# Kernel tuning notes

Hardware: AMD Instinct MI355X
Metric: run time of the kernel (lower is better)

Reference implementation:

```python
import jax, jax.numpy as jnp
import numpy as np

RADIUS = 1.0
BUMP = 32          # config.bump_steps
SCALE = 100.0      # sigmoid sharpness in compute_ecc
G = 32             # num_graphs

N, E, F = 16000, 48000, 32000
DIM, NDIR = 3, 64
HID, NC = 256, 10


def compute_ecc(h, index, lin):
    # h: [M, D]; lin: [BUMP] thresholds; index: [M] graph ids
    # sigmoid(scale * (lin - h)) broadcast -> [M, BUMP, D], segment-sum over M
    ecc = jax.nn.sigmoid(SCALE * (lin[None, :, None] - h[:, None, :]))
    return jax.ops.segment_sum(ecc, index, num_segments=G)  # [G, BUMP, D]


def setup_inputs() -> dict:
    key = jax.random.key(0)
    ks = jax.random.split(key, 12)
    x = jax.random.normal(ks[0], (N, DIM), dtype=jnp.float32)
    node_weights = jax.random.uniform(ks[1], (N,), dtype=jnp.float32)
    edge_weights = jax.random.uniform(ks[2], (E,), dtype=jnp.float32)
    face_weights = jax.random.uniform(ks[3], (F,), dtype=jnp.float32)
    v = jax.random.normal(ks[4], (DIM, NDIR), dtype=jnp.float32)
    v = v / jnp.linalg.norm(v, axis=0, keepdims=True)  # unit directions
    W1 = jax.random.normal(ks[5], (HID, NDIR * BUMP), dtype=jnp.float32) * 0.02
    b1 = jnp.zeros((HID,), dtype=jnp.float32)
    W2 = jax.random.normal(ks[6], (NC, HID), dtype=jnp.float32) * 0.02
    b2 = jnp.zeros((NC,), dtype=jnp.float32)
    edge_index = jax.random.randint(ks[7], (2, E), 0, N, dtype=jnp.int64)
    face = jax.random.randint(ks[8], (3, F), 0, N, dtype=jnp.int64)
    batch_ids = jnp.sort(jax.random.randint(ks[9], (N,), 0, G, dtype=jnp.int64))
    return {"x": x, "node_weights": node_weights, "edge_weights": edge_weights,
            "face_weights": face_weights, "v": v, "W1": W1, "b1": b1,
            "W2": W2, "b2": b2, "edge_index": edge_index, "face": face,
            "batch_ids": batch_ids}


def reference(x, node_weights, edge_weights, face_weights, v, W1, b1, W2, b2,
              edge_index, face, batch_ids):
    lin = jnp.linspace(-RADIUS, RADIUS, BUMP, dtype=jnp.float32)
    # node heights: weighted coords projected onto directions -> [N, D]
    nh = (x * node_weights[:, None]) @ v
    # edge heights: max over the 2 endpoints, then weight -> [E, D]
    eh = jnp.maximum(nh[edge_index[0]], nh[edge_index[1]]) * edge_weights[:, None]
    idx_e = batch_ids[edge_index[0]]
    # face heights: max over the 3 vertices -> [F, D]
    fh = jnp.max(nh[face], axis=0) * face_weights[:, None]
    idx_f = batch_ids[face[0]]
    ecc = compute_ecc(nh, batch_ids, lin)   # [G, BUMP, D]
    ecc = ecc - compute_ecc(eh, idx_e, lin)
    ecc = ecc + compute_ecc(fh, idx_f, lin)
    flat = ecc.reshape(G, -1)               # [G, BUMP*D]
    h = jax.nn.relu(flat @ W1.T + b1)
    logits = h @ W2.T + b2
    return (logits, flat)
```

## Files before the change

kernel.cpp:

```cpp
#include <hip/hip_runtime.h>
#include <hip/hip_bf16.h>

constexpr int NN = 16000, NE = 48000, NF = 32000;
constexpr int ND = 64, NB = 32, NG = 32;
constexpr int HIDN = 256, NCLS = 10;
constexpr int CHB = 32;
constexpr int EFB = (NE + NF + 255) / 256;
constexpr int PREB = EFB;
constexpr int CAPE = 4096, CAPF = 4096;
constexpr float KLOG = 144.26950408889634f;
constexpr float DLT  = 9.307710457348151f;
constexpr float INV_DLT = 0.10743849569269015f;
constexpr int HBINS = 39;

constexpr int ECCF_OFF = 0;
constexpr int CUR_OFF  = ECCF_OFF + NG * NB * ND;
constexpr int NOFS_OFF = CUR_OFF + 64;
constexpr int DONE_OFF = NOFS_OFF + 40;
constexpr int ER_OFF   = DONE_OFF + 32;
constexpr int FR_OFF   = ER_OFF + NG * CAPE * 8;
constexpr int HB_OFF   = FR_OFF + NG * CAPF * 12;
constexpr int ZERO_CNT = NG * NB * ND;

__device__ __forceinline__ int clamp_node(int n) {
    return ((unsigned)n < (unsigned)NN) ? n : 0;
}
template<bool BF> __device__ __forceinline__ float ldf(const void* p, int i) {
    return BF ? __bfloat162float(((const __hip_bfloat16*)p)[i]) : ((const float*)p)[i];
}
template<bool I64> __device__ __forceinline__ int ldi(const int* p, int i) {
    return I64 ? p[2 * i] : p[i];
}

__device__ __forceinline__ bool detect_bf(const void* xp) {
    const unsigned* xw = (const unsigned*)xp;
    unsigned w = xw[threadIdx.x & 63];
    return __ballot(((w >> 23) & 0xFFu) >= 200u) != 0ull;
}
__device__ __forceinline__ bool detect_i64(const int* eip) {
    const unsigned* eiw = (const unsigned*)eip;
    unsigned o = eiw[2 * (threadIdx.x & 63) + 1];
    return __ballot(o != 0u) == 0ull;
}

__device__ __forceinline__ float dot3w(float4 p, float v0, float v1, float v2) {
    return fmaf(p.z, v2, fmaf(p.y, v1, p.x * v0));
}

__device__ __forceinline__ void accum_hist(float h, float s, float* hb) {
    const float KDEC = __builtin_amdgcn_exp2f(-DLT);
    float hkL = fmaf(h, KLOG, KLOG);
    float fl = floorf((hkL - 14.0f) * INV_DLT);
    int jlo = (int)fl + 1;
    if (jlo >= 32) return;
    if (jlo < -4) { hb[4 * 64] += s; return; }
    float t0 = fmaf(-(fl + 1.0f), DLT, hkL);
    float e  = __builtin_amdgcn_exp2f(t0);
    float s0 = __builtin_amdgcn_rcpf(1.0f + e);  e *= KDEC;
    float s1 = __builtin_amdgcn_rcpf(1.0f + e);  e *= KDEC;
    float s2 = __builtin_amdgcn_rcpf(1.0f + e);
    float* p = hb + (jlo + 4) * 64;
    float v0 = p[0], v1 = p[64], v2 = p[128], v3 = p[192];
    p[0]   = v0 + s * s0;
    p[64]  = v1 + s * (s1 - s0);
    p[128] = v2 + s * (s2 - s1);
    p[192] = v3 + s * (1.0f - s2);
}

template<bool BF, bool I64>
__device__ __forceinline__ void pre_body(const void* x, const void* nw,
                                         const int* ei, const int* fc, const int* batch,
                                         const void* ew, const void* fw,
                                         float* wsf, int* wsi, unsigned* cur,
                                         float4* er4, float4* fr4,
                                         unsigned* cnt, unsigned* base) {
    int t = threadIdx.x;
    int gid = blockIdx.x * 256 + t;

    if (gid < ZERO_CNT / 4) {
        float4 z; z.x = z.y = z.z = z.w = 0.0f;
        *(float4*)(wsf + ECCF_OFF + gid * 4) = z;
    }

    if (blockIdx.x == 0 && t < 32)
        ((unsigned*)wsi)[DONE_OFF + t] = 0u;

    if (gid < NN) {
        int gn = ldi<I64>(batch, gid) & (NG - 1);
        int gp = (gid > 0) ? (ldi<I64>(batch, gid - 1) & (NG - 1)) : -1;
        for (int gg = gp + 1; gg <= gn; gg++) wsi[NOFS_OFF + gg] = gid;
        if (gid == NN - 1)
            for (int gg = gn + 1; gg <= NG; gg++) wsi[NOFS_OFF + gg] = NN;
    }

    {
        if (t < 64) cnt[t] = 0;
        __syncthreads();
        int id = gid;
        int bin = 0; unsigned rank = 0; bool act = false;
        if (id < NE + NF) {
            if (id < NE) bin = ldi<I64>(batch, clamp_node(ldi<I64>(ei, id))) & 31;
            else bin = 32 + (ldi<I64>(batch, clamp_node(ldi<I64>(fc, id - NE))) & 31);
            act = true;
            rank = atomicAdd(&cnt[bin], 1u);
        }
        __syncthreads();
        if (t < 64) base[t] = cnt[t] ? atomicAdd(&cur[t], cnt[t]) : 0u;
        __syncthreads();
        if (act) {
            int off = (int)(base[bin] + rank);
            if (bin < 32) {
                if (off < CAPE) {
                    int a = clamp_node(ldi<I64>(ei, id));
                    int b = clamp_node(ldi<I64>(ei, NE + id));
                    float wa = ldf<BF>(nw, a), wb = ldf<BF>(nw, b);
                    float4 ra, rb;
                    ra.x = ldf<BF>(x, 3*a)   * wa;
                    ra.y = ldf<BF>(x, 3*a+1) * wa;
                    ra.z = ldf<BF>(x, 3*a+2) * wa;
                    ra.w = ldf<BF>(ew, id);
                    rb.x = ldf<BF>(x, 3*b)   * wb;
                    rb.y = ldf<BF>(x, 3*b+1) * wb;
                    rb.z = ldf<BF>(x, 3*b+2) * wb;
                    rb.w = 0.0f;
                    float4* dst = er4 + ((size_t)bin * CAPE + off) * 2;
                    dst[0] = ra; dst[1] = rb;
                }
            } else {
                if (off < CAPF) {
                    int fid = id - NE;
                    int a = clamp_node(ldi<I64>(fc, fid));
                    int b = clamp_node(ldi<I64>(fc, NF + fid));
                    int c = clamp_node(ldi<I64>(fc, 2 * NF + fid));
                    float wa = ldf<BF>(nw, a), wb = ldf<BF>(nw, b), wc = ldf<BF>(nw, c);
                    float4 qa, qb, qc;
                    qa.x = ldf<BF>(x, 3*a)   * wa;
                    qa.y = ldf<BF>(x, 3*a+1) * wa;
                    qa.z = ldf<BF>(x, 3*a+2) * wa;
                    qa.w = ldf<BF>(fw, fid);
                    qb.x = ldf<BF>(x, 3*b)   * wb;
                    qb.y = ldf<BF>(x, 3*b+1) * wb;
                    qb.z = ldf<BF>(x, 3*b+2) * wb;
                    qb.w = 0.0f;
                    qc.x = ldf<BF>(x, 3*c)   * wc;
                    qc.y = ldf<BF>(x, 3*c+1) * wc;
                    qc.z = ldf<BF>(x, 3*c+2) * wc;
                    qc.w = 0.0f;
                    float4* dst = fr4 + ((size_t)(bin - 32) * CAPF + off) * 3;
                    dst[0] = qa; dst[1] = qb; dst[2] = qc;
                }
            }
        }
    }
}
__global__ __launch_bounds__(256) void k_pre(const void* __restrict__ x,
                                             const void* __restrict__ nw,
                                             const int* __restrict__ ei,
                                             const int* __restrict__ fc,
                                             const int* __restrict__ batch,
                                             const void* __restrict__ ew,
                                             const void* __restrict__ fw,
                                             float* __restrict__ wsf,
                                             int* __restrict__ wsi,
                                             unsigned* __restrict__ cur,
                                             float4* __restrict__ er4,
                                             float4* __restrict__ fr4) {
    __shared__ unsigned cnt[64], base[64];
    bool bf = detect_bf(x), i64 = detect_i64(ei);
    if (bf)  { if (i64) pre_body<true,true >(x,nw,ei,fc,batch,ew,fw,wsf,wsi,cur,er4,fr4,cnt,base);
               else     pre_body<true,false>(x,nw,ei,fc,batch,ew,fw,wsf,wsi,cur,er4,fr4,cnt,base); }
    else     { if (i64) pre_body<false,true >(x,nw,ei,fc,batch,ew,fw,wsf,wsi,cur,er4,fr4,cnt,base);
               else     pre_body<false,false>(x,nw,ei,fc,batch,ew,fw,wsf,wsi,cur,er4,fr4,cnt,base); }
}

template<bool BF>
__device__ __forceinline__ void ecc_body(const void* xx, const void* nw, const void* vv,
                                         const int* wsi, const unsigned* cur,
                                         float* eccf, const float4* er4,
                                         const float4* fr4, float* hist) {
    int t = threadIdx.x;
    int d = t & 63;
    int w = __builtin_amdgcn_readfirstlane(t) >> 6;
    int g  = blockIdx.x >> 5;
    int cb = blockIdx.x & (CHB - 1);
    int sid = cb * 4 + w;
    const int S = CHB * 4;

    float v0 = ldf<BF>(vv, d), v1 = ldf<BF>(vv, ND + d), v2 = ldf<BF>(vv, 2 * ND + d);

    float4* h4 = (float4*)hist;
    const int Q = HBINS * 16;
    float4 z; z.x = z.y = z.z = z.w = 0.0f;
    for (int j = t; j < 4 * Q; j += 256) h4[j] = z;
    __syncthreads();

    float* hb = hist + w * (HBINS * 64) + d;

    int ns = wsi[NOFS_OFF + g], nend = wsi[NOFS_OFF + g + 1];
    int i = ns + sid;
    for (; i + S < nend; i += 2 * S) {
        int j = i + S;
        float a0 = ldf<BF>(xx, 3*i), a1 = ldf<BF>(xx, 3*i+1), a2 = ldf<BF>(xx, 3*i+2);
        float wa = ldf<BF>(nw, i);
        float b0 = ldf<BF>(xx, 3*j), b1 = ldf<BF>(xx, 3*j+1), b2 = ldf<BF>(xx, 3*j+2);
        float wb = ldf<BF>(nw, j);
        accum_hist(fmaf(a2, v2, fmaf(a1, v1, a0 * v0)) * wa, 1.0f, hb);
        accum_hist(fmaf(b2, v2, fmaf(b1, v1, b0 * v0)) * wb, 1.0f, hb);
    }
    for (; i < nend; i += S) {
        float a0 = ldf<BF>(xx, 3*i), a1 = ldf<BF>(xx, 3*i+1), a2 = ldf<BF>(xx, 3*i+2);
        float wa = ldf<BF>(nw, i);
        accum_hist(fmaf(a2, v2, fmaf(a1, v1, a0 * v0)) * wa, 1.0f, hb);
    }

    int ecnt = min((int)cur[g], CAPE);
    const float4* eg = er4 + (size_t)g * CAPE * 2;
    i = sid;
    for (; i + S < ecnt; i += 2 * S) {
        float4 pa1 = eg[2*i],       pb1 = eg[2*i + 1];
        float4 pa2 = eg[2*(i+S)],   pb2 = eg[2*(i+S) + 1];
        float h1 = fmaxf(dot3w(pa1, v0, v1, v2), dot3w(pb1, v0, v1, v2)) * pa1.w;
        float h2 = fmaxf(dot3w(pa2, v0, v1, v2), dot3w(pb2, v0, v1, v2)) * pa2.w;
        accum_hist(h1, -1.0f, hb);
        accum_hist(h2, -1.0f, hb);
    }
    for (; i < ecnt; i += S) {
        float4 pa = eg[2*i], pb = eg[2*i + 1];
        accum_hist(fmaxf(dot3w(pa, v0, v1, v2), dot3w(pb, v0, v1, v2)) * pa.w,
                   -1.0f, hb);
    }

    int fcnt = min((int)cur[32 + g], CAPF);
    const float4* fg = fr4 + (size_t)g * CAPF * 3;
    i = sid;
    for (; i + S < fcnt; i += 2 * S) {
        float4 qa1 = fg[3*i], qb1 = fg[3*i + 1], qc1 = fg[3*i + 2];
        float4 qa2 = fg[3*(i+S)], qb2 = fg[3*(i+S) + 1], qc2 = fg[3*(i+S) + 2];
        float h1 = fmaxf(fmaxf(dot3w(qa1, v0, v1, v2), dot3w(qb1, v0, v1, v2)),
                         dot3w(qc1, v0, v1, v2)) * qa1.w;
        float h2 = fmaxf(fmaxf(dot3w(qa2, v0, v1, v2), dot3w(qb2, v0, v1, v2)),
                         dot3w(qc2, v0, v1, v2)) * qa2.w;
        accum_hist(h1, 1.0f, hb);
        accum_hist(h2, 1.0f, hb);
    }
    for (; i < fcnt; i += S) {
        float4 qa = fg[3*i], qb = fg[3*i + 1], qc = fg[3*i + 2];
        accum_hist(fmaxf(fmaxf(dot3w(qa, v0, v1, v2), dot3w(qb, v0, v1, v2)),
                         dot3w(qc, v0, v1, v2)) * qa.w, 1.0f, hb);
    }

    __syncthreads();
    for (int o = t; o < Q; o += 256) {
        float4 A = h4[o], B = h4[Q + o], C = h4[2*Q + o], D = h4[3*Q + o];
        A.x += B.x + C.x + D.x;  A.y += B.y + C.y + D.y;
        A.z += B.z + C.z + D.z;  A.w += B.w + C.w + D.w;
        h4[o] = A;
    }
    __syncthreads();
    {
        float* segw = hist + HBINS * 64;
        float run = 0.0f, pre[8];
#pragma unroll
        for (int jj = 0; jj < 8; jj++) {
            run += hist[(4 + w * 8 + jj) * 64 + d];
            pre[jj] = run;
        }
        float padb = hist[d] + hist[64 + d] + hist[128 + d] + hist[192 + d];
        segw[w * 64 + d] = run;
        __syncthreads();
        float base = padb;
#pragma unroll
        for (int u = 0; u < 3; u++) if (u < w) base += segw[u * 64 + d];
        float* eb = eccf + g * (NB * ND) + d;
#pragma unroll
        for (int jj = 0; jj < 8; jj++)
            unsafeAtomicAdd(eb + (w * 8 + jj) * 64, base + pre[jj]);
    }
}
__global__ __launch_bounds__(256, 4) void k_ecc(const void* __restrict__ x,
                                                const void* __restrict__ nw,
                                                const void* __restrict__ v,
                                                const int* __restrict__ wsi,
                                                const unsigned* __restrict__ cur,
                                                float* __restrict__ eccf,
                                                const float4* __restrict__ er4,
                                                const float4* __restrict__ fr4) {
    __shared__ float hist[4 * HBINS * 64];
    if (detect_bf(x)) ecc_body<true >(x, nw, v, wsi, cur, eccf, er4, fr4, hist);
    else              ecc_body<false>(x, nw, v, wsi, cur, eccf, er4, fr4, hist);
}

template<bool BF>
__device__ __forceinline__ void mlp_body(const void* W1, const void* b1,
                                         const void* W2, const void* b2,
                                         const float* eccf, float* hbuf,
                                         unsigned* done, void* outv,
                                         float* red, float* pr, unsigned* lastflag) {
    int g = blockIdx.x >> 3, hc = blockIdx.x & 7;
    int t = threadIdx.x;

    const float4* fp = (const float4*)(eccf + g * (NB * ND) + t * 8);
    float4 fa = fp[0], fb = fp[1];
    float fl[8] = {fa.x, fa.y, fa.z, fa.w, fb.x, fb.y, fb.z, fb.w};

    if (hc == 0) {
        int ob = NG * NCLS + g * (NB * ND) + t * 8;
        if (BF) {
#pragma unroll
            for (int j = 0; j < 8; j++)
                ((__hip_bfloat16*)outv)[ob + j] = __float2bfloat16(fl[j]);
        } else {
            ((float4*)((float*)outv + ob))[0] = fa;
            ((float4*)((float*)outv + ob))[1] = fb;
        }
    }

    float acc[32];
#pragma unroll
    for (int r = 0; r < 32; r++) acc[r] = 0.0f;
#pragma unroll 4
    for (int r = 0; r < 32; r++) {
        size_t wb = (size_t)(hc * 32 + r) * (NB * ND) + t * 8;
        float wv[8];
        if (BF) {
            uint4 u = *(const uint4*)((const __hip_bfloat16*)W1 + wb);
            wv[0] = __uint_as_float(u.x << 16); wv[1] = __uint_as_float(u.x & 0xffff0000u);
            wv[2] = __uint_as_float(u.y << 16); wv[3] = __uint_as_float(u.y & 0xffff0000u);
            wv[4] = __uint_as_float(u.z << 16); wv[5] = __uint_as_float(u.z & 0xffff0000u);
            wv[6] = __uint_as_float(u.w << 16); wv[7] = __uint_as_float(u.w & 0xffff0000u);
        } else {
            float4 a = *(const float4*)((const float*)W1 + wb);
            float4 b = *(const float4*)((const float*)W1 + wb + 4);
            wv[0]=a.x; wv[1]=a.y; wv[2]=a.z; wv[3]=a.w;
            wv[4]=b.x; wv[5]=b.y; wv[6]=b.z; wv[7]=b.w;
        }
        float s = 0.0f;
#pragma unroll
        for (int j = 0; j < 8; j++) s = fmaf(wv[j], fl[j], s);
        acc[r] = s;
    }

#pragma unroll
    for (int r = 0; r < 32; r++) red[t * 33 + r] = acc[r];
    __syncthreads();
    {
        int r = t >> 3, s8 = t & 7;
        float sum = 0.0f;
#pragma unroll
        for (int i = 0; i < 32; i++) sum += red[(s8 * 32 + i) * 33 + r];
        pr[r * 8 + s8] = sum;
    }
    __syncthreads();
    if (t < 32) {
        float h = ldf<BF>(b1, hc * 32 + t);
#pragma unroll
        for (int s8 = 0; s8 < 8; s8++) h += pr[t * 8 + s8];
        __hip_atomic_store(&hbuf[g * HIDN + hc * 32 + t], fmaxf(h, 0.0f),
                           __ATOMIC_RELAXED, __HIP_MEMORY_SCOPE_AGENT);
    }

    __syncthreads();
    if (t == 0) {
        unsigned prev = __hip_atomic_fetch_add(&done[g], 1u, __ATOMIC_RELAXED,
                                               __HIP_MEMORY_SCOPE_AGENT);
        *lastflag = (prev == 7u) ? 1u : 0u;
    }
    __syncthreads();
    if (*lastflag) {
        red[t] = __hip_atomic_load(&hbuf[g * HIDN + t], __ATOMIC_RELAXED,
                                   __HIP_MEMORY_SCOPE_AGENT);
        __syncthreads();
        int w = t >> 6, lane = t & 63;
        for (int c = w; c < NCLS; c += 4) {
            float p = red[lane]        * ldf<BF>(W2, c * HIDN + lane)
                    + red[lane + 64]   * ldf<BF>(W2, c * HIDN + lane + 64)
                    + red[lane + 128]  * ldf<BF>(W2, c * HIDN + lane + 128)
                    + red[lane + 192]  * ldf<BF>(W2, c * HIDN + lane + 192);
#pragma unroll
            for (int off = 32; off >= 1; off >>= 1) p += __shfl_xor(p, off);
            if (lane == 0) {
                float r = p + ldf<BF>(b2, c);
                if (BF) ((__hip_bfloat16*)outv)[g * NCLS + c] = __float2bfloat16(r);
                else    ((float*)outv)[g * NCLS + c] = r;
            }
        }
    }
}
__global__ __launch_bounds__(256) void k_mlp(const void* __restrict__ W1,
                                             const void* __restrict__ b1,
                                             const void* __restrict__ W2,
                                             const void* __restrict__ b2,
                                             const float* __restrict__ eccf,
                                             float* __restrict__ hbuf,
                                             unsigned* __restrict__ done,
                                             void* __restrict__ outv,
                                             const void* __restrict__ x) {
    __shared__ float red[256 * 33];
    __shared__ float pr[256];
    __shared__ unsigned lastflag;
    if (detect_bf(x)) mlp_body<true >(W1, b1, W2, b2, eccf, hbuf, done, outv, red, pr, &lastflag);
    else              mlp_body<false>(W1, b1, W2, b2, eccf, hbuf, done, outv, red, pr, &lastflag);
}

extern "C" void kernel_launch(void* const* d_in, const int* in_sizes, int n_in,
                              void* d_out, int out_size, void* d_ws, size_t ws_size,
                              hipStream_t stream) {
    const void* x  = d_in[0];
    const void* nw = d_in[1];
    const void* ew = d_in[2];
    const void* fw = d_in[3];
    const void* v  = d_in[4];
    const void* W1 = d_in[5];
    const void* b1 = d_in[6];
    const void* W2 = d_in[7];
    const void* b2 = d_in[8];
    const int* ei    = (const int*)d_in[9];
    const int* fc    = (const int*)d_in[10];
    const int* batch = (const int*)d_in[11];

    float*    wsf = (float*)d_ws;
    unsigned* wsu = (unsigned*)d_ws;
    int*      wsi = (int*)d_ws;
    float*    eccf = wsf + ECCF_OFF;
    unsigned* cur  = wsu + CUR_OFF;
    unsigned* done = wsu + DONE_OFF;
    float*    hbuf = wsf + HB_OFF;
    float4*   er4  = (float4*)(wsf + ER_OFF);
    float4*   fr4  = (float4*)(wsf + FR_OFF);

    hipMemsetAsync((char*)d_ws + (size_t)CUR_OFF * 4, 0, 64 * 4, stream);

    k_pre<<<PREB, 256, 0, stream>>>(x, nw, ei, fc, batch, ew, fw, wsf, wsi, cur, er4, fr4);
    k_ecc<<<NG * CHB, 256, 0, stream>>>(x, nw, v, wsi, cur, eccf, er4, fr4);
    k_mlp<<<NG * 8, 256, 0, stream>>>(W1, b1, W2, b2, eccf, hbuf, done, d_out, x);
}
```

Measured before the change: 118.6 us.

## Fuse MLP stage into ECC kernel with per-graph completion counter spin-wait

Removes the separate MLP kernel launch. Each ECC block drains its atomics and bumps a per-graph done counter. The first 8 chunk blocks of each graph then spin until all 32 blocks have finished and run the MLP chunk, reusing the histogram shared memory. The counters are now cleared by a wider memset, and a second counter handles the final-layer reduction. This relies on all 1024 blocks being co-resident to avoid deadlock, and it adds spin-wait latency on the critical blocks.

```diff
diff --git a/kernel.cpp b/kernel.cpp
--- a/kernel.cpp
+++ b/kernel.cpp
@@ -17,10 +17,12 @@
 constexpr int CUR_OFF  = ECCF_OFF + NG * NB * ND;
 constexpr int NOFS_OFF = CUR_OFF + 64;
 constexpr int DONE_OFF = NOFS_OFF + 40;
-constexpr int ER_OFF   = DONE_OFF + 32;
+constexpr int DONE2_OFF= DONE_OFF + 32;
+constexpr int ER_OFF   = DONE2_OFF + 32;
 constexpr int FR_OFF   = ER_OFF + NG * CAPE * 8;
 constexpr int HB_OFF   = FR_OFF + NG * CAPF * 12;
 constexpr int ZERO_CNT = NG * NB * ND;
+constexpr int MS_WORDS = 168;
 
 __device__ __forceinline__ int clamp_node(int n) {
     return ((unsigned)n < (unsigned)NN) ? n : 0;
@@ -81,9 +83,6 @@
         float4 z; z.x = z.y = z.z = z.w = 0.0f;
         *(float4*)(wsf + ECCF_OFF + gid * 4) = z;
     }
-
-    if (blockIdx.x == 0 && t < 32)
-        ((unsigned*)wsi)[DONE_OFF + t] = 0u;
 
     if (gid < NN) {
         int gn = ldi<I64>(batch, gid) & (NG - 1);
@@ -174,134 +173,20 @@
 }
 
 template<bool BF>
-__device__ __forceinline__ void ecc_body(const void* xx, const void* nw, const void* vv,
-                                         const int* wsi, const unsigned* cur,
-                                         float* eccf, const float4* er4,
-                                         const float4* fr4, float* hist) {
+__device__ __forceinline__ void mlp_chunk(int g, int hc, const void* W1, const void* b1,
+                                          const void* W2, const void* b2,
+                                          const float* eccf, float* hbuf,
+                                          unsigned* done2, void* outv,
+                                          float* red, float* pr, unsigned* lastflag) {
     int t = threadIdx.x;
-    int d = t & 63;
-    int w = __builtin_amdgcn_readfirstlane(t) >> 6;
-    int g  = blockIdx.x >> 5;
-    int cb = blockIdx.x & (CHB - 1);
-    int sid = cb * 4 + w;
-    const int S = CHB * 4;
-
-    float v0 = ldf<BF>(vv, d), v1 = ldf<BF>(vv, ND + d), v2 = ldf<BF>(vv, 2 * ND + d);
-
-    float4* h4 = (float4*)hist;
-    const int Q = HBINS * 16;
-    float4 z; z.x = z.y = z.z = z.w = 0.0f;
-    for (int j = t; j < 4 * Q; j += 256) h4[j] = z;
-    __syncthreads();
-
-    float* hb = hist + w * (HBINS * 64) + d;
-
-    int ns = wsi[NOFS_OFF + g], nend = wsi[NOFS_OFF + g + 1];
-    int i = ns + sid;
-    for (; i + S < nend; i += 2 * S) {
-        int j = i + S;
-        float a0 = ldf<BF>(xx, 3*i), a1 = ldf<BF>(xx, 3*i+1), a2 = ldf<BF>(xx, 3*i+2);
-        float wa = ldf<BF>(nw, i);
-        float b0 = ldf<BF>(xx, 3*j), b1 = ldf<BF>(xx, 3*j+1), b2 = ldf<BF>(xx, 3*j+2);
-        float wb = ldf<BF>(nw, j);
-        accum_hist(fmaf(a2, v2, fmaf(a1, v1, a0 * v0)) * wa, 1.0f, hb);
-        accum_hist(fmaf(b2, v2, fmaf(b1, v1, b0 * v0)) * wb, 1.0f, hb);
-    }
-    for (; i < nend; i += S) {
-        float a0 = ldf<BF>(xx, 3*i), a1 = ldf<BF>(xx, 3*i+1), a2 = ldf<BF>(xx, 3*i+2);
-        float wa = ldf<BF>(nw, i);
-        accum_hist(fmaf(a2, v2, fmaf(a1, v1, a0 * v0)) * wa, 1.0f, hb);
-    }
-
-    int ecnt = min((int)cur[g], CAPE);
-    const float4* eg = er4 + (size_t)g * CAPE * 2;
-    i = sid;
-    for (; i + S < ecnt; i += 2 * S) {
-        float4 pa1 = eg[2*i],       pb1 = eg[2*i + 1];
-        float4 pa2 = eg[2*(i+S)],   pb2 = eg[2*(i+S) + 1];
-        float h1 = fmaxf(dot3w(pa1, v0, v1, v2), dot3w(pb1, v0, v1, v2)) * pa1.w;
-        float h2 = fmaxf(dot3w(pa2, v0, v1, v2), dot3w(pb2, v0, v1, v2)) * pa2.w;
-        accum_hist(h1, -1.0f, hb);
-        accum_hist(h2, -1.0f, hb);
-    }
-    for (; i < ecnt; i += S) {
-        float4 pa = eg[2*i], pb = eg[2*i + 1];
-        accum_hist(fmaxf(dot3w(pa, v0, v1, v2), dot3w(pb, v0, v1, v2)) * pa.w,
-                   -1.0f, hb);
-    }
-
-    int fcnt = min((int)cur[32 + g], CAPF);
-    const float4* fg = fr4 + (size_t)g * CAPF * 3;
-    i = sid;
-    for (; i + S < fcnt; i += 2 * S) {
-        float4 qa1 = fg[3*i], qb1 = fg[3*i + 1], qc1 = fg[3*i + 2];
-        float4 qa2 = fg[3*(i+S)], qb2 = fg[3*(i+S) + 1], qc2 = fg[3*(i+S) + 2];
-        float h1 = fmaxf(fmaxf(dot3w(qa1, v0, v1, v2), dot3w(qb1, v0, v1, v2)),
-                         dot3w(qc1, v0, v1, v2)) * qa1.w;
-        float h2 = fmaxf(fmaxf(dot3w(qa2, v0, v1, v2), dot3w(qb2, v0, v1, v2)),
-                         dot3w(qc2, v0, v1, v2)) * qa2.w;
-        accum_hist(h1, 1.0f, hb);
-        accum_hist(h2, 1.0f, hb);
-    }
-    for (; i < fcnt; i += S) {
-        float4 qa = fg[3*i], qb = fg[3*i + 1], qc = fg[3*i + 2];
-        accum_hist(fmaxf(fmaxf(dot3w(qa, v0, v1, v2), dot3w(qb, v0, v1, v2)),
-                         dot3w(qc, v0, v1, v2)) * qa.w, 1.0f, hb);
-    }
-
-    __syncthreads();
-    for (int o = t; o < Q; o += 256) {
-        float4 A = h4[o], B = h4[Q + o], C = h4[2*Q + o], D = h4[3*Q + o];
-        A.x += B.x + C.x + D.x;  A.y += B.y + C.y + D.y;
-        A.z += B.z + C.z + D.z;  A.w += B.w + C.w + D.w;
-        h4[o] = A;
-    }
-    __syncthreads();
-    {
-        float* segw = hist + HBINS * 64;
-        float run = 0.0f, pre[8];
-#pragma unroll
-        for (int jj = 0; jj < 8; jj++) {
-            run += hist[(4 + w * 8 + jj) * 64 + d];
-            pre[jj] = run;
-        }
-        float padb = hist[d] + hist[64 + d] + hist[128 + d] + hist[192 + d];
-        segw[w * 64 + d] = run;
-        __syncthreads();
-        float base = padb;
-#pragma unroll
-        for (int u = 0; u < 3; u++) if (u < w) base += segw[u * 64 + d];
-        float* eb = eccf + g * (NB * ND) + d;
-#pragma unroll
-        for (int jj = 0; jj < 8; jj++)
-            unsafeAtomicAdd(eb + (w * 8 + jj) * 64, base + pre[jj]);
-    }
-}
-__global__ __launch_bounds__(256, 4) void k_ecc(const void* __restrict__ x,
-                                                const void* __restrict__ nw,
-                                                const void* __restrict__ v,
-                                                const int* __restrict__ wsi,
-                                                const unsigned* __restrict__ cur,
-                                                float* __restrict__ eccf,
-                                                const float4* __restrict__ er4,
-                                                const float4* __restrict__ fr4) {
-    __shared__ float hist[4 * HBINS * 64];
-    if (detect_bf(x)) ecc_body<true >(x, nw, v, wsi, cur, eccf, er4, fr4, hist);
-    else              ecc_body<false>(x, nw, v, wsi, cur, eccf, er4, fr4, hist);
-}
-
-template<bool BF>
-__device__ __forceinline__ void mlp_body(const void* W1, const void* b1,
-                                         const void* W2, const void* b2,
-                                         const float* eccf, float* hbuf,
-                                         unsigned* done, void* outv,
-                                         float* red, float* pr, unsigned* lastflag) {
-    int g = blockIdx.x >> 3, hc = blockIdx.x & 7;
-    int t = threadIdx.x;
-
-    const float4* fp = (const float4*)(eccf + g * (NB * ND) + t * 8);
-    float4 fa = fp[0], fb = fp[1];
-    float fl[8] = {fa.x, fa.y, fa.z, fa.w, fb.x, fb.y, fb.z, fb.w};
+
+    float fl[8];
+#pragma unroll
+    for (int j = 0; j < 8; j++) {
+        unsigned uv = __hip_atomic_load((const unsigned*)&eccf[g * (NB * ND) + t * 8 + j],
+                                        __ATOMIC_RELAXED, __HIP_MEMORY_SCOPE_AGENT);
+        fl[j] = __uint_as_float(uv);
+    }
 
     if (hc == 0) {
         int ob = NG * NCLS + g * (NB * ND) + t * 8;
@@ -310,8 +195,9 @@
             for (int j = 0; j < 8; j++)
                 ((__hip_bfloat16*)outv)[ob + j] = __float2bfloat16(fl[j]);
         } else {
-            ((float4*)((float*)outv + ob))[0] = fa;
-            ((float4*)((float*)outv + ob))[1] = fb;
+#pragma unroll
+            for (int j = 0; j < 8; j++)
+                ((float*)outv)[ob + j] = fl[j];
         }
     }
 
@@ -361,7 +247,7 @@
 
     __syncthreads();
     if (t == 0) {
-        unsigned prev = __hip_atomic_fetch_add(&done[g], 1u, __ATOMIC_RELAXED,
+        unsigned prev = __hip_atomic_fetch_add(&done2[g], 1u, __ATOMIC_RELAXED,
                                                __HIP_MEMORY_SCOPE_AGENT);
         *lastflag = (prev == 7u) ? 1u : 0u;
     }
@@ -386,20 +272,157 @@
         }
     }
 }
-__global__ __launch_bounds__(256) void k_mlp(const void* __restrict__ W1,
-                                             const void* __restrict__ b1,
-                                             const void* __restrict__ W2,
-                                             const void* __restrict__ b2,
-                                             const float* __restrict__ eccf,
-                                             float* __restrict__ hbuf,
-                                             unsigned* __restrict__ done,
-                                             void* __restrict__ outv,
-                                             const void* __restrict__ x) {
-    __shared__ float red[256 * 33];
-    __shared__ float pr[256];
+
+template<bool BF>
+__device__ __forceinline__ void ecc_body(const void* xx, const void* nw, const void* vv,
+                                         const int* wsi, const unsigned* cur,
+                                         float* eccf, const float4* er4,
+                                         const float4* fr4, float* hist,
+                                         const void* W1, const void* b1,
+                                         const void* W2, const void* b2,
+                                         float* hbuf, unsigned* done,
+                                         unsigned* done2, void* outv,
+                                         unsigned* lastflag) {
+    int t = threadIdx.x;
+    int d = t & 63;
+    int w = __builtin_amdgcn_readfirstlane(t) >> 6;
+    int g  = blockIdx.x >> 5;
+    int cb = blockIdx.x & (CHB - 1);
+    int sid = cb * 4 + w;
+    const int S = CHB * 4;
+
+    float v0 = ldf<BF>(vv, d), v1 = ldf<BF>(vv, ND + d), v2 = ldf<BF>(vv, 2 * ND + d);
+
+    float4* h4 = (float4*)hist;
+    const int Q = HBINS * 16;
+    float4 z; z.x = z.y = z.z = z.w = 0.0f;
+    for (int j = t; j < 4 * Q; j += 256) h4[j] = z;
+    __syncthreads();
+
+    float* hb = hist + w * (HBINS * 64) + d;
+
+    int ns = wsi[NOFS_OFF + g], nend = wsi[NOFS_OFF + g + 1];
+    int i = ns + sid;
+    for (; i + S < nend; i += 2 * S) {
+        int j = i + S;
+        float a0 = ldf<BF>(xx, 3*i), a1 = ldf<BF>(xx, 3*i+1), a2 = ldf<BF>(xx, 3*i+2);
+        float wa = ldf<BF>(nw, i);
+        float b0 = ldf<BF>(xx, 3*j), b1v = ldf<BF>(xx, 3*j+1), b2v = ldf<BF>(xx, 3*j+2);
+        float wb = ldf<BF>(nw, j);
+        accum_hist(fmaf(a2, v2, fmaf(a1, v1, a0 * v0)) * wa, 1.0f, hb);
+        accum_hist(fmaf(b2v, v2, fmaf(b1v, v1, b0 * v0)) * wb, 1.0f, hb);
+    }
+    for (; i < nend; i += S) {
+        float a0 = ldf<BF>(xx, 3*i), a1 = ldf<BF>(xx, 3*i+1), a2 = ldf<BF>(xx, 3*i+2);
+        float wa = ldf<BF>(nw, i);
+        accum_hist(fmaf(a2, v2, fmaf(a1, v1, a0 * v0)) * wa, 1.0f, hb);
+    }
+
+    int ecnt = min((int)cur[g], CAPE);
+    const float4* eg = er4 + (size_t)g * CAPE * 2;
+    i = sid;
+    for (; i + S < ecnt; i += 2 * S) {
+        float4 pa1 = eg[2*i],       pb1 = eg[2*i + 1];
+        float4 pa2 = eg[2*(i+S)],   pb2 = eg[2*(i+S) + 1];
+        float h1 = fmaxf(dot3w(pa1, v0, v1, v2), dot3w(pb1, v0, v1, v2)) * pa1.w;
+        float h2 = fmaxf(dot3w(pa2, v0, v1, v2), dot3w(pb2, v0, v1, v2)) * pa2.w;
+        accum_hist(h1, -1.0f, hb);
+        accum_hist(h2, -1.0f, hb);
+    }
+    for (; i < ecnt; i += S) {
+        float4 pa = eg[2*i], pb = eg[2*i + 1];
+        accum_hist(fmaxf(dot3w(pa, v0, v1, v2), dot3w(pb, v0, v1, v2)) * pa.w,
+                   -1.0f, hb);
+    }
+
+    int fcnt = min((int)cur[32 + g], CAPF);
+    const float4* fg = fr4 + (size_t)g * CAPF * 3;
+    i = sid;
+    for (; i + S < fcnt; i += 2 * S) {
+        float4 qa1 = fg[3*i], qb1 = fg[3*i + 1], qc1 = fg[3*i + 2];
+        float4 qa2 = fg[3*(i+S)], qb2 = fg[3*(i+S) + 1], qc2 = fg[3*(i+S) + 2];
+        float h1 = fmaxf(fmaxf(dot3w(qa1, v0, v1, v2), dot3w(qb1, v0, v1, v2)),
+                         dot3w(qc1, v0, v1, v2)) * qa1.w;
+        float h2 = fmaxf(fmaxf(dot3w(qa2, v0, v1, v2), dot3w(qb2, v0, v1, v2)),
+                         dot3w(qc2, v0, v1, v2)) * qa2.w;
+        accum_hist(h1, 1.0f, hb);
+        accum_hist(h2, 1.0f, hb);
+    }
+    for (; i < fcnt; i += S) {
+        float4 qa = fg[3*i], qb = fg[3*i + 1], qc = fg[3*i + 2];
+        accum_hist(fmaxf(fmaxf(dot3w(qa, v0, v1, v2), dot3w(qb, v0, v1, v2)),
+                         dot3w(qc, v0, v1, v2)) * qa.w, 1.0f, hb);
+    }
+
+    __syncthreads();
+    for (int o = t; o < Q; o += 256) {
+        float4 A = h4[o], B = h4[Q + o], C = h4[2*Q + o], D = h4[3*Q + o];
+        A.x += B.x + C.x + D.x;  A.y += B.y + C.y + D.y;
+        A.z += B.z + C.z + D.z;  A.w += B.w + C.w + D.w;
+        h4[o] = A;
+    }
+    __syncthreads();
+    {
+        float* segw = hist + HBINS * 64;
+        float run = 0.0f, pre[8];
+#pragma unroll
+        for (int jj = 0; jj < 8; jj++) {
+            run += hist[(4 + w * 8 + jj) * 64 + d];
+            pre[jj] = run;
+        }
+        float padb = hist[d] + hist[64 + d] + hist[128 + d] + hist[192 + d];
+        segw[w * 64 + d] = run;
+        __syncthreads();
+        float base = padb;
+#pragma unroll
+        for (int u = 0; u < 3; u++) if (u < w) base += segw[u * 64 + d];
+        float* eb = eccf + g * (NB * ND) + d;
+#pragma unroll
+        for (int jj = 0; jj < 8; jj++)
+            unsafeAtomicAdd(eb + (w * 8 + jj) * 64, base + pre[jj]);
+    }
+
+    asm volatile("s_waitcnt vmcnt(0)" ::: "memory");
+    __syncthreads();
+    if (t == 0) {
+        __hip_atomic_fetch_add(&done[g], 1u, __ATOMIC_RELAXED,
+                               __HIP_MEMORY_SCOPE_AGENT);
+    }
+    if (cb < 8) {
+        if (t == 0) {
+            for (int it = 0; it < (1 << 24); ++it) {
+                if (__hip_atomic_load(&done[g], __ATOMIC_RELAXED,
+                                      __HIP_MEMORY_SCOPE_AGENT) >= 32u) break;
+                __builtin_amdgcn_s_sleep(2);
+            }
+        }
+        __syncthreads();
+        mlp_chunk<BF>(g, cb, W1, b1, W2, b2, eccf, hbuf, done2, outv,
+                      hist, hist + 8448, lastflag);
+    }
+}
+__global__ __launch_bounds__(256, 4) void k_ecc(const void* __restrict__ x,
+                                                const void* __restrict__ nw,
+                                                const void* __restrict__ v,
+                                                const int* __restrict__ wsi,
+                                                const unsigned* __restrict__ cur,
+                                                float* __restrict__ eccf,
+                                                const float4* __restrict__ er4,
+                                                const float4* __restrict__ fr4,
+                                                const void* __restrict__ W1,
+                                                const void* __restrict__ b1,
+                                                const void* __restrict__ W2,
+                                                const void* __restrict__ b2,
+                                                float* __restrict__ hbuf,
+                                                unsigned* __restrict__ done,
+                                                unsigned* __restrict__ done2,
+                                                void* __restrict__ outv) {
+    __shared__ float hist[4 * HBINS * 64];
     __shared__ unsigned lastflag;
-    if (detect_bf(x)) mlp_body<true >(W1, b1, W2, b2, eccf, hbuf, done, outv, red, pr, &lastflag);
-    else              mlp_body<false>(W1, b1, W2, b2, eccf, hbuf, done, outv, red, pr, &lastflag);
+    if (detect_bf(x)) ecc_body<true >(x, nw, v, wsi, cur, eccf, er4, fr4, hist,
+                                      W1, b1, W2, b2, hbuf, done, done2, outv, &lastflag);
+    else              ecc_body<false>(x, nw, v, wsi, cur, eccf, er4, fr4, hist,
+                                      W1, b1, W2, b2, hbuf, done, done2, outv, &lastflag);
 }
 
 extern "C" void kernel_launch(void* const* d_in, const int* in_sizes, int n_in,
@@ -424,13 +447,14 @@
     float*    eccf = wsf + ECCF_OFF;
     unsigned* cur  = wsu + CUR_OFF;
     unsigned* done = wsu + DONE_OFF;
+    unsigned* done2= wsu + DONE2_OFF;
     float*    hbuf = wsf + HB_OFF;
     float4*   er4  = (float4*)(wsf + ER_OFF);
     float4*   fr4  = (float4*)(wsf + FR_OFF);
 
-    hipMemsetAsync((char*)d_ws + (size_t)CUR_OFF * 4, 0, 64 * 4, stream);
+    hipMemsetAsync((char*)d_ws + (size_t)CUR_OFF * 4, 0, MS_WORDS * 4, stream);
 
     k_pre<<<PREB, 256, 0, stream>>>(x, nw, ei, fc, batch, ew, fw, wsf, wsi, cur, er4, fr4);
-    k_ecc<<<NG * CHB, 256, 0, stream>>>(x, nw, v, wsi, cur, eccf, er4, fr4);
-    k_mlp<<<NG * 8, 256, 0, stream>>>(W1, b1, W2, b2, eccf, hbuf, done, d_out, x);
-}
+    k_ecc<<<NG * CHB, 256, 0, stream>>>(x, nw, v, wsi, cur, eccf, er4, fr4,
+                                        W1, b1, W2, b2, hbuf, done, done2, d_out);
+}
```

After: 138.2 us. 1.17x slower.
